# Kernel tuning notes

Hardware: AMD Instinct MI355X
Metric: run time of the kernel (lower is better)

Reference implementation:

```python
import jax, jax.numpy as jnp
import numpy as np

# --- constants (UnscaleSST / SST range assumed; see notes) ---
SST_MEAN = 13.5
SST_STD = 8.0
SST_MIN = -2.0
SST_MAX = 35.0
WIN = 11          # pytorch-msssim default gaussian window size
SIGMA = 1.5       # default gaussian sigma
K1, K2 = 0.01, 0.03
DATA_RANGE = 1.0


def _gauss_win():
    coords = np.arange(WIN, dtype=np.float64) - WIN // 2
    g = np.exp(-(coords ** 2) / (2.0 * SIGMA ** 2))
    g = g / g.sum()
    return jnp.asarray(g, dtype=jnp.float32)


def _blur(x, g):
    # separable valid-padding gaussian filter, NCHW single channel
    dn = ('NCHW', 'OIHW', 'NCHW')
    kh = g.reshape(1, 1, WIN, 1)
    kw = g.reshape(1, 1, 1, WIN)
    x = jax.lax.conv_general_dilated(x, kh, (1, 1), 'VALID', dimension_numbers=dn)
    x = jax.lax.conv_general_dilated(x, kw, (1, 1), 'VALID', dimension_numbers=dn)
    return x


def _unnormalize(x):
    x = x * SST_STD + SST_MEAN               # UnscaleSST (inverse standardization)
    x = (x - SST_MIN) / (SST_MAX - SST_MIN)  # min-max to [0, 1]
    return jnp.nan_to_num(x)


def _ssim(X, Y):
    g = _gauss_win()
    C1 = (K1 * DATA_RANGE) ** 2
    C2 = (K2 * DATA_RANGE) ** 2
    mu1 = _blur(X, g)
    mu2 = _blur(Y, g)
    mu1_sq, mu2_sq, mu12 = mu1 * mu1, mu2 * mu2, mu1 * mu2
    sigma1_sq = _blur(X * X, g) - mu1_sq
    sigma2_sq = _blur(Y * Y, g) - mu2_sq
    sigma12 = _blur(X * Y, g) - mu12
    cs_map = (2.0 * sigma12 + C2) / (sigma1_sq + sigma2_sq + C2)
    ssim_map = ((2.0 * mu12 + C1) / (mu1_sq + mu2_sq + C1)) * cs_map
    # per-channel mean over spatial dims -> [B, C]
    ssim_pc = ssim_map.mean(axis=(2, 3))
    ssim_pc = jax.nn.relu(ssim_pc)  # nonnegative_ssim=True
    return ssim_pc.mean()           # size_average=True


def setup_inputs() -> dict:
    key = jax.random.key(0)
    k1, k2 = jax.random.split(key)
    shape = (64, 1, 512, 512)
    pred = jax.random.normal(k1, shape, dtype=jnp.float32)
    target = jax.random.normal(k2, shape, dtype=jnp.float32)
    return {"pred": pred, "target": target}


def reference(pred, target):
    return _ssim(_unnormalize(pred), _unnormalize(target))
```

## Files before the change

### kernel.cpp

```cpp
#include <hip/hip_runtime.h>
#include <math.h>


typedef float v2f __attribute__((ext_vector_type(2)));

#define WIN 11
#define IMG 512
#define OUTW 502
#define BAND 64
#define RY 8
#define NCHUNK (BAND / RY)
#define COLS2 514

constexpr float A_SC  = 8.0f / 37.0f;
constexpr float TWO_B = 2.0f * (15.5f / 37.0f);
constexpr float TWO_C1 = 2.0f * 1e-4f;
constexpr float TWO_C2 = 2.0f * 9e-4f;

__global__ __launch_bounds__(512, 4)
void ssim_main(const float* __restrict__ X, const float* __restrict__ Y,
               float* __restrict__ ws)
{
    __shared__ __align__(16) v2f sP[2][RY][COLS2];
    __shared__ float sW[WIN];
    __shared__ float sRed[8];

    const int tid  = threadIdx.x;
    const int band = blockIdx.x;
    const int b    = blockIdx.y;
    const int y0   = band * BAND;

    if (tid == 0) {
        double g[WIN]; double sum = 0.0;
        for (int k = 0; k < WIN; ++k) { double c = k - 5; g[k] = exp(-(c * c) / 4.5); sum += g[k]; }
        for (int k = 0; k < WIN; ++k) sW[k] = (float)(g[k] / sum);
    }
    if (tid < 32) {
        const int pp = tid >> 4;
        const int rr = (tid >> 1) & 7;
        const int cc = 512 + (tid & 1);
        sP[pp][rr][cc] = (v2f)0.0f;
    }
    __syncthreads();
    float w[WIN];
    #pragma unroll
    for (int k = 0; k < WIN; ++k)
        w[k] = __uint_as_float(__builtin_amdgcn_readfirstlane(__float_as_uint(sW[k])));

    const float* __restrict__ Xb = X + (size_t)b * (IMG * (size_t)IMG);
    const float* __restrict__ Yb = Y + (size_t)b * (IMG * (size_t)IMG);

    const int x  = tid;
    const int hr = tid & 7;
    const int cg = tid >> 3;
    const int x0 = cg << 3;

    float acc = 0.0f;

    v2f psd[10];
    #pragma unroll
    for (int i = 0; i < 10; ++i) {
        const uint32_t idx = (uint32_t)(y0 + i) * IMG + (uint32_t)x;
        const float xv = Xb[idx], yv = Yb[idx];
        v2f t; t.x = fmaf(xv + yv, A_SC, TWO_B); t.y = (xv - yv) * A_SC;
        psd[i] = t;
    }

    #pragma unroll 1
    for (int c = -1; c < NCHUNK; ++c) {
        const int vchunk = c + 1;
        const bool dovert = (vchunk < NCHUNK);
        const int nbase = y0 + vchunk * RY;

        float fx[RY], fy[RY];
        if (dovert) {
            #pragma unroll
            for (int jj = 0; jj < RY; ++jj) {
                int yi = nbase + 10 + jj; yi = yi < IMG - 1 ? yi : IMG - 1;
                const uint32_t idx = (uint32_t)yi * IMG + (uint32_t)x;
                fx[jj] = Xb[idx]; fy[jj] = Yb[idx];
            }
        }

        if (c >= 0) {
            const int yo = y0 + c * RY + hr;
            if (yo < OUTW && x0 < OUTW) {
                v2f Hacc[2][8];
                #pragma unroll
                for (int p = 0; p < 2; ++p) {
                    #pragma unroll
                    for (int i = 0; i < 8; ++i) Hacc[p][i] = (v2f)0.0f;
                    const float4* q4 = (const float4*)&sP[p][hr][x0];
                    #pragma unroll
                    for (int j4 = 0; j4 < 9; ++j4) {
                        const float4 qq = q4[j4];
                        #pragma unroll
                        for (int h = 0; h < 2; ++h) {
                            const int e = 2 * j4 + h;
                            v2f col; col.x = h ? qq.z : qq.x; col.y = h ? qq.w : qq.y;
                            #pragma unroll
                            for (int i = 0; i < 8; ++i) {
                                const int k = e - i;
                                if (k >= 0 && k < WIN) Hacc[p][i] += w[k] * col;
                            }
                        }
                    }
                }
                #pragma unroll
                for (int i = 0; i < 8; ++i) {
                    if (x0 + i < OUTW) {
                        const v2f m2 = Hacc[0][i] * Hacc[0][i];
                        const v2f sg = Hacc[1][i] - m2;
                        const float t1 = m2.x + TWO_C1;
                        const float na = t1 - m2.y;
                        const float da = t1 + m2.y;
                        const float t2 = sg.x + TWO_C2;
                        const float nb = t2 - sg.y;
                        const float db = t2 + sg.y;
                        acc = fmaf(na * nb, __builtin_amdgcn_rcpf(da * db), acc);
                    }
                }
            }
        }

        if (dovert) {
            v2f vsd[RY], vq[RY];
            #pragma unroll
            for (int rr = 0; rr < RY; ++rr) { vsd[rr] = (v2f)0.0f; vq[rr] = (v2f)0.0f; }

            #pragma unroll
            for (int j = 0; j < 10; ++j) {
                const v2f a = psd[j];
                const v2f q = a * a;
                #pragma unroll
                for (int rr = 0; rr < RY; ++rr) {
                    const int k = j - rr;
                    if (k >= 0 && k < WIN) {
                        const float wk = w[k];
                        vsd[rr] += wk * a;
                        vq[rr]  += wk * q;
                    }
                }
            }
            psd[0] = psd[8];
            psd[1] = psd[9];
            #pragma unroll
            for (int jj = 0; jj < RY; ++jj) {
                const int j = 10 + jj;
                v2f a; a.x = fmaf(fx[jj] + fy[jj], A_SC, TWO_B); a.y = (fx[jj] - fy[jj]) * A_SC;
                const v2f q = a * a;
                #pragma unroll
                for (int rr = 0; rr < RY; ++rr) {
                    const int k = j - rr;
                    if (k >= 0 && k < WIN) {
                        const float wk = w[k];
                        vsd[rr] += wk * a;
                        vq[rr]  += wk * q;
                    }
                }
                psd[2 + jj] = a;
            }

            if (c >= 0) __syncthreads();

            #pragma unroll
            for (int rr = 0; rr < RY; ++rr) {
                sP[0][rr][x] = vsd[rr];
                sP[1][rr][x] = vq[rr];
            }
            __syncthreads();
        }
    }

    #pragma unroll
    for (int off = 32; off > 0; off >>= 1) acc += __shfl_down(acc, off, 64);
    if ((tid & 63) == 0) sRed[tid >> 6] = acc;
    __syncthreads();
    if (tid == 0) {
        float t = 0.f;
        #pragma unroll
        for (int i = 0; i < 8; ++i) t += sRed[i];
        atomicAdd(&ws[b], t);
    }
}

__global__ void ssim_finalize(const float* __restrict__ ws, float* __restrict__ out)
{
    const int t = threadIdx.x;
    float v = ws[t] * (1.0f / (502.0f * 502.0f));
    v = v > 0.f ? v : 0.f;
    #pragma unroll
    for (int off = 32; off > 0; off >>= 1) v += __shfl_down(v, off, 64);
    if (t == 0) out[0] = v * (1.0f / 64.0f);
}

extern "C" void kernel_launch(void* const* d_in, const int* in_sizes, int n_in,
                              void* d_out, int out_size, void* d_ws, size_t ws_size,
                              hipStream_t stream)
{
    const float* pred   = (const float*)d_in[0];
    const float* target = (const float*)d_in[1];
    float* out = (float*)d_out;
    float* ws  = (float*)d_ws;

    ssim_main<<<dim3(8, 64), 512, 0, stream>>>(pred, target, ws);
    ssim_finalize<<<1, 64, 0, stream>>>(ws, out);
}
```

Measured before the change: 157.9 us.

## Split SSIM work into 128-wide column tiles and 32-row bands

Replaces full-width 512-thread bands of 64 rows with 128-thread blocks covering 118-output-column tiles (with a 10-column halo) and 32-row bands. This raises the grid from 512 to 5120 blocks, giving more parallelism and smaller blocks with cheaper barriers. The cost is redundant halo work: about 8% extra columns loaded and vertically filtered per tile, plus more vertical-halo rows per band. The sync placement was also restructured.

```diff
diff --git a/kernel.cpp b/kernel.cpp
--- a/kernel.cpp
+++ b/kernel.cpp
@@ -7,28 +7,35 @@
 #define WIN 11
 #define IMG 512
 #define OUTW 502
-#define BAND 64
+#define BAND 32
 #define RY 8
 #define NCHUNK (BAND / RY)
-#define COLS2 514
+#define TILE_OUT 118
+#define TILE_LD  128
+#define COLT 130
+#define NTX 5
+#define NBY 16
 
 constexpr float A_SC  = 8.0f / 37.0f;
 constexpr float TWO_B = 2.0f * (15.5f / 37.0f);
 constexpr float TWO_C1 = 2.0f * 1e-4f;
 constexpr float TWO_C2 = 2.0f * 9e-4f;
 
-__global__ __launch_bounds__(512, 4)
+__global__ __launch_bounds__(128, 4)
 void ssim_main(const float* __restrict__ X, const float* __restrict__ Y,
                float* __restrict__ ws)
 {
-    __shared__ __align__(16) v2f sP[2][RY][COLS2];
+    __shared__ __align__(16) v2f sP[2][RY][COLT];
     __shared__ float sW[WIN];
-    __shared__ float sRed[8];
+    __shared__ float sRed[2];
 
     const int tid  = threadIdx.x;
-    const int band = blockIdx.x;
+    const int bx   = blockIdx.x;
+    const int tx   = bx >> 4;
+    const int band = bx & 15;
     const int b    = blockIdx.y;
     const int y0   = band * BAND;
+    const int xT   = tx * TILE_OUT;
 
     if (tid == 0) {
         double g[WIN]; double sum = 0.0;
@@ -36,9 +43,7 @@
         for (int k = 0; k < WIN; ++k) sW[k] = (float)(g[k] / sum);
     }
     if (tid < 32) {
-        const int pp = tid >> 4;
-        const int rr = (tid >> 1) & 7;
-        const int cc = 512 + (tid & 1);
+        const int pp = tid >> 4, rr = (tid >> 1) & 7, cc = 128 + (tid & 1);
         sP[pp][rr][cc] = (v2f)0.0f;
     }
     __syncthreads();
@@ -50,17 +55,17 @@
     const float* __restrict__ Xb = X + (size_t)b * (IMG * (size_t)IMG);
     const float* __restrict__ Yb = Y + (size_t)b * (IMG * (size_t)IMG);
 
-    const int x  = tid;
+    const int gcol = min(xT + tid, IMG - 1);
     const int hr = tid & 7;
-    const int cg = tid >> 3;
-    const int x0 = cg << 3;
+    const int cgH = tid >> 3;
+    const int c0 = cgH << 3;
 
     float acc = 0.0f;
 
     v2f psd[10];
     #pragma unroll
     for (int i = 0; i < 10; ++i) {
-        const uint32_t idx = (uint32_t)(y0 + i) * IMG + (uint32_t)x;
+        const uint32_t idx = (uint32_t)(y0 + i) * IMG + (uint32_t)gcol;
         const float xv = Xb[idx], yv = Yb[idx];
         v2f t; t.x = fmaf(xv + yv, A_SC, TWO_B); t.y = (xv - yv) * A_SC;
         psd[i] = t;
@@ -77,20 +82,20 @@
             #pragma unroll
             for (int jj = 0; jj < RY; ++jj) {
                 int yi = nbase + 10 + jj; yi = yi < IMG - 1 ? yi : IMG - 1;
-                const uint32_t idx = (uint32_t)yi * IMG + (uint32_t)x;
+                const uint32_t idx = (uint32_t)yi * IMG + (uint32_t)gcol;
                 fx[jj] = Xb[idx]; fy[jj] = Yb[idx];
             }
         }
 
-        if (c >= 0) {
+        if (c >= 0 && c0 <= 112) {
             const int yo = y0 + c * RY + hr;
-            if (yo < OUTW && x0 < OUTW) {
+            if (yo < OUTW) {
                 v2f Hacc[2][8];
                 #pragma unroll
                 for (int p = 0; p < 2; ++p) {
                     #pragma unroll
                     for (int i = 0; i < 8; ++i) Hacc[p][i] = (v2f)0.0f;
-                    const float4* q4 = (const float4*)&sP[p][hr][x0];
+                    const float4* q4 = (const float4*)&sP[p][hr][c0];
                     #pragma unroll
                     for (int j4 = 0; j4 < 9; ++j4) {
                         const float4 qq = q4[j4];
@@ -108,7 +113,8 @@
                 }
                 #pragma unroll
                 for (int i = 0; i < 8; ++i) {
-                    if (x0 + i < OUTW) {
+                    const int lc = c0 + i;
+                    if (lc < TILE_OUT && xT + lc < OUTW) {
                         const v2f m2 = Hacc[0][i] * Hacc[0][i];
                         const v2f sg = Hacc[1][i] - m2;
                         const float t1 = m2.x + TWO_C1;
@@ -123,11 +129,10 @@
             }
         }
 
+        v2f vsd[RY], vq[RY];
         if (dovert) {
-            v2f vsd[RY], vq[RY];
             #pragma unroll
             for (int rr = 0; rr < RY; ++rr) { vsd[rr] = (v2f)0.0f; vq[rr] = (v2f)0.0f; }
-
             #pragma unroll
             for (int j = 0; j < 10; ++j) {
                 const v2f a = psd[j];
@@ -135,7 +140,7 @@
                 #pragma unroll
                 for (int rr = 0; rr < RY; ++rr) {
                     const int k = j - rr;
-                    if (k >= 0 && k < WIN) {
+                    if (k >= 0) {
                         const float wk = w[k];
                         vsd[rr] += wk * a;
                         vq[rr]  += wk * q;
@@ -152,7 +157,7 @@
                 #pragma unroll
                 for (int rr = 0; rr < RY; ++rr) {
                     const int k = j - rr;
-                    if (k >= 0 && k < WIN) {
+                    if (k <= 10) {
                         const float wk = w[k];
                         vsd[rr] += wk * a;
                         vq[rr]  += wk * q;
@@ -160,13 +165,15 @@
                 }
                 psd[2 + jj] = a;
             }
-
-            if (c >= 0) __syncthreads();
-
+        }
+
+        if (c >= 0 && dovert) __syncthreads();
+
+        if (dovert) {
             #pragma unroll
             for (int rr = 0; rr < RY; ++rr) {
-                sP[0][rr][x] = vsd[rr];
-                sP[1][rr][x] = vq[rr];
+                sP[0][rr][tid] = vsd[rr];
+                sP[1][rr][tid] = vq[rr];
             }
             __syncthreads();
         }
@@ -176,12 +183,7 @@
     for (int off = 32; off > 0; off >>= 1) acc += __shfl_down(acc, off, 64);
     if ((tid & 63) == 0) sRed[tid >> 6] = acc;
     __syncthreads();
-    if (tid == 0) {
-        float t = 0.f;
-        #pragma unroll
-        for (int i = 0; i < 8; ++i) t += sRed[i];
-        atomicAdd(&ws[b], t);
-    }
+    if (tid == 0) atomicAdd(&ws[b], sRed[0] + sRed[1]);
 }
 
 __global__ void ssim_finalize(const float* __restrict__ ws, float* __restrict__ out)
@@ -203,6 +205,6 @@
     float* out = (float*)d_out;
     float* ws  = (float*)d_ws;
 
-    ssim_main<<<dim3(8, 64), 512, 0, stream>>>(pred, target, ws);
+    ssim_main<<<dim3(NTX * NBY, 64), 128, 0, stream>>>(pred, target, ws);
     ssim_finalize<<<1, 64, 0, stream>>>(ws, out);
 }
```

New measurement: 262.2 us. 66.1% more time.
